# Kernel optimization log

Hardware: AMD Instinct MI355X
Metric: run time of the kernel (lower is better)

Reference implementation:

```python
import jax, jax.numpy as jnp
import numpy as np

TAU = 2.0
V_TH = 1.0
V_RST = 0.0
BN_EPS = 1e-5

# --- ATan surrogate-gradient Heaviside spike (spikingjelly default, alpha=2) ---
@jax.custom_vjp
def atan_spike(x):
    return (x >= 0.0).astype(x.dtype)

def _atan_fwd(x):
    return atan_spike(x), x

def _atan_bwd(x, g):
    alpha = 2.0
    return (g * (alpha / 2.0) / (1.0 + (jnp.pi / 2.0 * alpha * x) ** 2),)

atan_spike.defvjp(_atan_fwd, _atan_bwd)

# --- multi-step LIF (decay_input=False, hard reset, detach_reset=True) ---
def lif(x_seq):
    def step(v, xt):
        v = v - (v - V_RST) / TAU + xt            # charge
        s = atan_spike(v - V_TH)                  # fire
        sd = jax.lax.stop_gradient(s)             # detach_reset
        v = (1.0 - sd) * v + sd * V_RST           # hard reset
        return v, s
    v0 = jnp.full(x_seq.shape[1:], V_RST, x_seq.dtype)
    _, spikes = jax.lax.scan(step, v0, x_seq)
    return spikes

def setup_inputs() -> dict:
    key = jax.random.key(0)
    k1, k2 = jax.random.split(key)
    T, B, N = 64, 256, 512
    x = jax.random.normal(k1, (T, B, N), dtype=jnp.float32)
    # xavier-uniform-like init for Linear weight [out, in]
    bound = float(np.sqrt(6.0 / (N + N)))
    W = jax.random.uniform(k2, (N, N), minval=-bound, maxval=bound, dtype=jnp.float32)
    gamma = jnp.ones((N,), jnp.float32)
    beta = jnp.zeros((N,), jnp.float32)
    return {"x": x, "W": W, "gamma": gamma, "beta": beta}

def reference(x, W, gamma, beta):
    # x: [T, B, N]
    T, B, N = x.shape
    # spatial / temporal spiking gates (reduction='mean')
    spatial = lif(x.mean(axis=-1, keepdims=True))   # [T, B, 1]
    temporal = lif(x.mean(axis=0, keepdims=True))   # [1, B, N] (scan over length-1 T)
    s = (x * spatial) * (x * temporal)
    x = x + s
    x = lif(x)
    # Linear (no bias): y = x @ W.T
    x = jnp.einsum('tbn,mn->tbm', x, W)
    # BatchNorm1d over channels N, stats over flattened T*B (training mode)
    xf = x.reshape(T * B, N)
    mu = xf.mean(axis=0)
    var = xf.var(axis=0)
    xf = (xf - mu) * jax.lax.rsqrt(var + BN_EPS) * gamma + beta
    x = xf.reshape(T, B, N)
    x = lif(x)
    return x
```

## Files before the change

kernel.cpp:

```cpp
#include <hip/hip_runtime.h>
#include <hip/hip_bf16.h>
#include <math.h>

#define TT 64
#define BB 256
#define NN 512

typedef int i32x4  __attribute__((ext_vector_type(4)));
typedef int i32x16 __attribute__((ext_vector_type(16)));

__device__ __forceinline__ void gload16(const void* g, void* l) {
  __builtin_amdgcn_global_load_lds(
      (const __attribute__((address_space(1))) unsigned int*)g,
      (__attribute__((address_space(3))) unsigned int*)l, 16, 0, 0);
}

__global__ __launch_bounds__(256) void wprep_kernel(
    const float* __restrict__ W, signed char* __restrict__ wd) {
  int i = blockIdx.x * 256 + threadIdx.x;
  float v = W[i];
  int q = __float2int_rn(v * 1073741824.0f);
  int d0 = ((q + 128) & 255) - 128; q = (q - d0) >> 8;
  int d1 = ((q + 128) & 255) - 128; q = (q - d1) >> 8;
  int d2 = ((q + 128) & 255) - 128; q = (q - d2) >> 8;
  wd[i]          = (signed char)d0;
  wd[262144 + i] = (signed char)d1;
  wd[524288 + i] = (signed char)d2;
  wd[786432 + i] = (signed char)q;
}

__global__ __launch_bounds__(512) void frontend_kernel(
    const float* __restrict__ x, unsigned char* __restrict__ spk) {
  extern __shared__ float xs[];
  __shared__ float rms[TT];
  __shared__ float sp[TT];
  int b = blockIdx.x, tid = threadIdx.x;
  int l = tid & 63, w = tid >> 6;
  #pragma unroll
  for (int p = 0; p < 16; ++p) {
    int f = p * 512 + tid;
    int t = f >> 7, c4 = f & 127;
    gload16(x + (size_t)t * (BB * NN) + (size_t)b * NN + c4 * 4,
            (char*)xs + p * 8192 + w * 1024);
  }
  __syncthreads();
  #pragma unroll
  for (int j = 0; j < 8; ++j) {
    int t = w * 8 + j;
    float s = 0.f;
    #pragma unroll
    for (int q = 0; q < 8; ++q) s += xs[t * 512 + q * 64 + l];
    #pragma unroll
    for (int off = 32; off; off >>= 1) s += __shfl_xor(s, off);
    if (l == 0) rms[t] = s;
  }
  float cs = 0.f;
  for (int t = 0; t < TT; ++t) cs += xs[t * 512 + tid];
  __syncthreads();
  if (tid == 0) {
    float v = 0.f;
    for (int t = 0; t < TT; ++t) {
      float m = rms[t] * (1.0f / 512.0f);
      v = v - v * 0.5f + m;
      float s = (v >= 1.0f) ? 1.0f : 0.0f;
      sp[t] = s;
      if (s != 0.f) v = 0.f;
    }
  }
  __syncthreads();
  float te = (cs * (1.0f / 64.0f) >= 1.0f) ? 1.0f : 0.0f;
  float v = 0.f;
  unsigned char* sb = spk + (size_t)b * NN + tid;
  for (int t = 0; t < TT; ++t) {
    float xv = xs[t * 512 + tid];
    float a = xv + (xv * sp[t]) * (xv * te);
    v = v - v * 0.5f + a;
    unsigned char s = (v >= 1.0f) ? 1 : 0;
    sb[(size_t)t * (BB * NN)] = s;
    if (s) v = 0.f;
  }
}

__global__ __launch_bounds__(256) void gemm_kernel(
    const unsigned char* __restrict__ A, const signed char* __restrict__ Wd,
    float* __restrict__ C, float* __restrict__ pS, float* __restrict__ pQ) {
  __shared__ unsigned char sm[2][24576];
  int tid = threadIdx.x;
  int l = tid & 63, w = tid >> 6;
  int wr = w >> 1, wc = w & 1;
  int bx = blockIdx.x, by = blockIdx.y;
  int row0 = bx * 128, col0 = by * 64;
  int lr = l & 31, lh = l >> 5;

  i32x16 acc[2][4];
  #pragma unroll
  for (int f = 0; f < 2; ++f)
    #pragma unroll
    for (int d = 0; d < 4; ++d)
      #pragma unroll
      for (int j = 0; j < 16; ++j) acc[f][d][j] = 0;

  auto STAGE = [&](unsigned char* lbase, int kk) {
    #pragma unroll
    for (int j = 0; j < 2; ++j) {
      int c = j * 4 + w;
      int wr_ = c >> 2, ff = (c >> 1) & 1, ss = c & 1;
      gload16(A + (size_t)(row0 + wr_ * 64 + ff * 32 + lr) * NN + kk + ss * 32 + lh * 16,
              lbase + j * 4096 + w * 1024);
    }
    #pragma unroll
    for (int j = 0; j < 4; ++j) {
      int c = j * 4 + w;
      int wc_ = c >> 3, dd = (c >> 1) & 3, ss = c & 1;
      gload16(Wd + (size_t)dd * (NN * NN) + (size_t)(col0 + wc_ * 32 + lr) * NN + kk + ss * 32 + lh * 16,
              lbase + 8192 + j * 4096 + w * 1024);
    }
  };

  STAGE(sm[0], 0);
  __syncthreads();
  int cur = 0;
  for (int t = 0; t < 8; ++t) {
    if (t < 7) STAGE(sm[cur ^ 1], (t + 1) * 64);
    const unsigned char* bp = sm[cur];
    i32x4 a[2][2], bfr[4][2];
    #pragma unroll
    for (int f = 0; f < 2; ++f)
      #pragma unroll
      for (int s = 0; s < 2; ++s)
        a[f][s] = *(const i32x4*)(bp + ((wr * 2 + f) * 2 + s) * 1024 + l * 16);
    #pragma unroll
    for (int d = 0; d < 4; ++d)
      #pragma unroll
      for (int s = 0; s < 2; ++s)
        bfr[d][s] = *(const i32x4*)(bp + 8192 + ((wc * 4 + d) * 2 + s) * 1024 + l * 16);
    #pragma unroll
    for (int s = 0; s < 2; ++s)
      #pragma unroll
      for (int f = 0; f < 2; ++f)
        #pragma unroll
        for (int d = 0; d < 4; ++d)
          acc[f][d] = __builtin_amdgcn_mfma_i32_32x32x32_i8(a[f][s], bfr[d][s], acc[f][d], 0, 0, 0);
    __syncthreads();
    cur ^= 1;
  }

  int col = col0 + wc * 32 + lr;
  float sy = 0.f, sq = 0.f;
  #pragma unroll
  for (int f = 0; f < 2; ++f) {
    #pragma unroll
    for (int j = 0; j < 16; ++j) {
      int t2 = acc[f][2][j] + (acc[f][3][j] << 8);
      int t1 = acc[f][1][j] + (t2 << 8);
      long long tt = ((long long)t1 << 8) + (long long)acc[f][0][j];
      float y = (float)tt * 0x1p-30f;
      int row = row0 + wr * 64 + f * 32 + (j & 3) + 8 * (j >> 2) + 4 * lh;
      C[(size_t)row * NN + col] = y;
      sy += y; sq += y * y;
    }
  }
  sy += __shfl_xor(sy, 32);
  sq += __shfl_xor(sq, 32);
  if (lh == 0) {
    pS[(size_t)col * 256 + bx * 2 + wr] = sy;
    pQ[(size_t)col * 256 + bx * 2 + wr] = sq;
  }
}

__global__ __launch_bounds__(512) void bnstatsB_kernel(
    const float* __restrict__ pS, const float* __restrict__ pQ,
    float* __restrict__ mu, float* __restrict__ inv) {
  int tid = threadIdx.x;
  int ch = blockIdx.x * 64 + (tid >> 3), p = tid & 7;
  const float* ps = pS + (size_t)ch * 256 + p * 32;
  const float* pq = pQ + (size_t)ch * 256 + p * 32;
  float s = 0.f, q = 0.f;
  #pragma unroll
  for (int i = 0; i < 32; ++i) { s += ps[i]; q += pq[i]; }
  #pragma unroll
  for (int off = 1; off < 8; off <<= 1) { s += __shfl_xor(s, off); q += __shfl_xor(q, off); }
  if (p == 0) {
    float mean = s * (1.0f / 16384.0f);
    float var  = q * (1.0f / 16384.0f) - mean * mean;
    mu[ch] = mean;
    inv[ch] = 1.0f / sqrtf(var + 1e-5f);
  }
}

__global__ __launch_bounds__(256) void final_kernel(
    float* __restrict__ y, const float* __restrict__ mu, const float* __restrict__ inv,
    const float* __restrict__ gamma, const float* __restrict__ beta) {
  int g = blockIdx.x * 256 + threadIdx.x;
  int b = g >> 9, m = g & 511;
  float MU = mu[m], IV = inv[m], G = gamma[m], BE = beta[m];
  float* p = y + (size_t)b * NN + m;
  const size_t st = (size_t)BB * NN;
  float buf[16], nxt[16];
  #pragma unroll
  for (int j = 0; j < 16; ++j) buf[j] = p[(size_t)j * st];
  float v = 0.f;
  #pragma unroll
  for (int t0 = 0; t0 < 64; t0 += 16) {
    if (t0 + 16 < 64) {
      #pragma unroll
      for (int j = 0; j < 16; ++j) nxt[j] = p[(size_t)(t0 + 16 + j) * st];
    }
    #pragma unroll
    for (int j = 0; j < 16; ++j) {
      float xb = (buf[j] - MU) * IV * G + BE;
      v = v - v * 0.5f + xb;
      float s = (v >= 1.0f) ? 1.0f : 0.0f;
      p[(size_t)(t0 + j) * st] = s;
      if (s != 0.f) v = 0.f;
    }
    #pragma unroll
    for (int j = 0; j < 16; ++j) buf[j] = nxt[j];
  }
}

extern "C" void kernel_launch(void* const* d_in, const int* in_sizes, int n_in,
                              void* d_out, int out_size, void* d_ws, size_t ws_size,
                              hipStream_t stream) {
  const float* x     = (const float*)d_in[0];
  const float* W     = (const float*)d_in[1];
  const float* gamma = (const float*)d_in[2];
  const float* beta  = (const float*)d_in[3];
  float* out = (float*)d_out;

  char* ws = (char*)d_ws;
  signed char* wd       = (signed char*)ws;
  unsigned char* spikes = (unsigned char*)(ws + 1048576);
  float* pS    = (float*)(ws + 9437184);
  float* pQ    = (float*)(ws + 9961472);
  float* bn_mu = (float*)(ws + 10485760);
  float* bn_inv= (float*)(ws + 10487808);

  wprep_kernel<<<dim3(1024), dim3(256), 0, stream>>>(W, wd);
  frontend_kernel<<<dim3(BB), dim3(512), 131072, stream>>>(x, spikes);
  gemm_kernel<<<dim3(128, 8), dim3(256), 0, stream>>>(spikes, wd, out, pS, pQ);
  bnstatsB_kernel<<<dim3(8), dim3(512), 0, stream>>>(pS, pQ, bn_mu, bn_inv);
  final_kernel<<<dim3(512), dim3(256), 0, stream>>>(out, bn_mu, bn_inv, gamma, beta);
}
```

Before: 152.5 us.

## Triple-buffer GEMM loads with manual waitcnt barriers and parallelize spatial LIF

Result: faster. 146.6 us (-3.9%).

```diff
diff --git a/kernel.cpp b/kernel.cpp
--- a/kernel.cpp
+++ b/kernel.cpp
@@ -57,15 +57,17 @@
   float cs = 0.f;
   for (int t = 0; t < TT; ++t) cs += xs[t * 512 + tid];
   __syncthreads();
-  if (tid == 0) {
+  if (w == 0) {
+    float myrm = rms[l];
     float v = 0.f;
+    unsigned long long mask = 0ull;
+    #pragma unroll
     for (int t = 0; t < TT; ++t) {
-      float m = rms[t] * (1.0f / 512.0f);
-      v = v - v * 0.5f + m;
-      float s = (v >= 1.0f) ? 1.0f : 0.0f;
-      sp[t] = s;
-      if (s != 0.f) v = 0.f;
-    }
+      float m = __shfl(myrm, t) * (1.0f / 512.0f);
+      v = v * 0.5f + m;
+      if (v >= 1.0f) { mask |= (1ull << t); v = 0.f; }
+    }
+    sp[l] = (float)((mask >> l) & 1ull);
   }
   __syncthreads();
   float te = (cs * (1.0f / 64.0f) >= 1.0f) ? 1.0f : 0.0f;
@@ -74,7 +76,7 @@
   for (int t = 0; t < TT; ++t) {
     float xv = xs[t * 512 + tid];
     float a = xv + (xv * sp[t]) * (xv * te);
-    v = v - v * 0.5f + a;
+    v = v * 0.5f + a;
     unsigned char s = (v >= 1.0f) ? 1 : 0;
     sb[(size_t)t * (BB * NN)] = s;
     if (s) v = 0.f;
@@ -84,7 +86,7 @@
 __global__ __launch_bounds__(256) void gemm_kernel(
     const unsigned char* __restrict__ A, const signed char* __restrict__ Wd,
     float* __restrict__ C, float* __restrict__ pS, float* __restrict__ pQ) {
-  __shared__ unsigned char sm[2][24576];
+  __shared__ unsigned char sm[3][24576];
   int tid = threadIdx.x;
   int l = tid & 63, w = tid >> 6;
   int wr = w >> 1, wc = w & 1;
@@ -118,11 +120,15 @@
   };
 
   STAGE(sm[0], 0);
-  __syncthreads();
-  int cur = 0;
+  STAGE(sm[1], 64);
+  #pragma unroll
   for (int t = 0; t < 8; ++t) {
-    if (t < 7) STAGE(sm[cur ^ 1], (t + 1) * 64);
-    const unsigned char* bp = sm[cur];
+    asm volatile("s_waitcnt lgkmcnt(0)" ::: "memory");
+    if (t < 7) asm volatile("s_waitcnt vmcnt(6)" ::: "memory");
+    else       asm volatile("s_waitcnt vmcnt(0)" ::: "memory");
+    asm volatile("s_barrier" ::: "memory");
+    if (t < 6) STAGE(sm[(t + 2) % 3], (t + 2) * 64);
+    const unsigned char* bp = sm[t % 3];
     i32x4 a[2][2], bfr[4][2];
     #pragma unroll
     for (int f = 0; f < 2; ++f)
@@ -134,6 +140,7 @@
       #pragma unroll
       for (int s = 0; s < 2; ++s)
         bfr[d][s] = *(const i32x4*)(bp + 8192 + ((wc * 4 + d) * 2 + s) * 1024 + l * 16);
+    __builtin_amdgcn_s_setprio(1);
     #pragma unroll
     for (int s = 0; s < 2; ++s)
       #pragma unroll
@@ -141,8 +148,7 @@
         #pragma unroll
         for (int d = 0; d < 4; ++d)
           acc[f][d] = __builtin_amdgcn_mfma_i32_32x32x32_i8(a[f][s], bfr[d][s], acc[f][d], 0, 0, 0);
-    __syncthreads();
-    cur ^= 1;
+    __builtin_amdgcn_s_setprio(0);
   }
 
   int col = col0 + wc * 32 + lr;
@@ -209,7 +215,7 @@
     #pragma unroll
     for (int j = 0; j < 16; ++j) {
       float xb = (buf[j] - MU) * IV * G + BE;
-      v = v - v * 0.5f + xb;
+      v = v * 0.5f + xb;
       float s = (v >= 1.0f) ? 1.0f : 0.0f;
       p[(size_t)(t0 + j) * st] = s;
       if (s != 0.f) v = 0.f;
```
